# Performance work log

Measured on AMD Instinct MI355X. Metric: run time of the kernel, lower is better.

## Reference

```python
import jax, jax.numpy as jnp
import numpy as np

N, E, H = 50000, 800000, 4

def setup_inputs() -> dict:
    key = jax.random.key(0)
    ks = jax.random.split(key, 16)
    feat = jax.random.normal(ks[0], (N, 2), dtype=jnp.float32)
    src = jax.random.randint(ks[1], (E,), 0, N, dtype=jnp.int32)
    dst = jax.random.randint(ks[2], (E,), 0, N, dtype=jnp.int32)
    def w(k, shape, fan_in):
        return jax.random.normal(k, shape, dtype=jnp.float32) * (1.0 / np.sqrt(fan_in))
    # layer 1: 2 -> 4 heads x 32
    W1 = w(ks[3], (2, 128), 2); al1 = w(ks[4], (H, 32), 32); ar1 = w(ks[5], (H, 32), 32); b1 = jnp.zeros((128,), jnp.float32)
    # layer 2: 128 -> 4 heads x 32
    W2 = w(ks[6], (128, 128), 128); al2 = w(ks[7], (H, 32), 32); ar2 = w(ks[8], (H, 32), 32); b2 = jnp.zeros((128,), jnp.float32)
    # layer 3: 128 -> 4 heads x 64
    W3 = w(ks[9], (128, 256), 128); al3 = w(ks[10], (H, 64), 64); ar3 = w(ks[11], (H, 64), 64); b3 = jnp.zeros((256,), jnp.float32)
    return dict(feat=feat, src=src, dst=dst, W1=W1, al1=al1, ar1=ar1, b1=b1,
                W2=W2, al2=al2, ar2=ar2, b2=b2, W3=W3, al3=al3, ar3=ar3, b3=b3)

def gat_layer(h, W, al, ar, b, src, dst):
    # h: [N, Fin]; W: [Fin, H*D]; al/ar: [H, D]; b: [H*D]
    Hh, D = al.shape
    z = (h @ W).reshape(-1, Hh, D)                      # [N, H, D]
    el = jnp.sum(z * al[None], axis=-1)                 # [N, H]
    er = jnp.sum(z * ar[None], axis=-1)                 # [N, H]
    e = jax.nn.leaky_relu(el[src] + er[dst], 0.2)       # [E, H]
    m = jax.ops.segment_max(e, dst, num_segments=N)     # [N, H] per-dst max
    ex = jnp.exp(e - m[dst])                            # [E, H]
    s = jax.ops.segment_sum(ex, dst, num_segments=N)    # [N, H]
    alpha = ex / s[dst]                                 # edge softmax
    msg = z[src] * alpha[:, :, None]                    # [E, H, D] gathered+weighted
    out = jax.ops.segment_sum(msg, dst, num_segments=N) # [N, H, D]
    return out.reshape(N, Hh * D) + b

def reference(feat, src, dst, W1, al1, ar1, b1, W2, al2, ar2, b2, W3, al3, ar3, b3):
    # dropout is identity at inference
    h = jax.nn.relu(gat_layer(feat, W1, al1, ar1, b1, src, dst))
    h = jax.nn.relu(gat_layer(h, W2, al2, ar2, b2, src, dst))
    h = gat_layer(h, W3, al3, ar3, b3, src, dst)
    return h
```

## Files before the change

### kernel.cpp

```cpp
#include <hip/hip_runtime.h>
#include <math.h>


#define NEG_BIG (-1e38f)

typedef _Float16 h8 __attribute__((ext_vector_type(8)));
typedef _Float16 h4 __attribute__((ext_vector_type(4)));

static inline int cdiv(int a, int b) { return (a + b - 1) / b; }

__device__ __forceinline__ float lrelu(float x) { return (x >= 0.f) ? x : 0.2f * x; }


__global__ void count_deg_kernel(const int* __restrict__ dst, int* __restrict__ deg, int E) {
    int i = blockIdx.x * blockDim.x + threadIdx.x;
    if (i < E) atomicAdd(&deg[dst[i]], 1);
}

__global__ __launch_bounds__(256) void scan1_kernel(const int* __restrict__ deg,
                                                    int* __restrict__ rowptr,
                                                    int* __restrict__ bsum, int n) {
    __shared__ int wsum[4];
    int t = threadIdx.x;
    int l = t & 63, wv = t >> 6;
    int i = blockIdx.x * 256 + t;
    int v = (i < n) ? deg[i] : 0;
    int x = v;
    #pragma unroll
    for (int off = 1; off < 64; off <<= 1) {
        int y = __shfl_up(x, off);
        if (l >= off) x += y;
    }
    if (l == 63) wsum[wv] = x;
    __syncthreads();
    int wo = 0;
    #pragma unroll
    for (int j = 0; j < 4; ++j)
        if (j < wv) wo += wsum[j];
    if (i < n) rowptr[i] = wo + x - v;
    if (t == 255) bsum[blockIdx.x] = wo + x;
}

__global__ __launch_bounds__(256) void scan2_kernel(const int* __restrict__ bsum,
                                                    int* __restrict__ boff, int nb) {
    __shared__ int wsum[4];
    int t = threadIdx.x;
    int l = t & 63, wv = t >> 6;
    int v = (t < nb) ? bsum[t] : 0;
    int x = v;
    #pragma unroll
    for (int off = 1; off < 64; off <<= 1) {
        int y = __shfl_up(x, off);
        if (l >= off) x += y;
    }
    if (l == 63) wsum[wv] = x;
    __syncthreads();
    int wo = 0;
    #pragma unroll
    for (int j = 0; j < 4; ++j)
        if (j < wv) wo += wsum[j];
    if (t < nb) boff[t] = wo + x - v;
}

__global__ __launch_bounds__(256) void scan3_kernel(int* __restrict__ rowptr,
                                                    const int* __restrict__ boff,
                                                    int n, int E) {
    int i = blockIdx.x * 256 + threadIdx.x;
    if (i < n) rowptr[i] += boff[blockIdx.x];
    if (i == 0) rowptr[n] = E;
}

__global__ void fill_csr_kernel(const int* __restrict__ src, const int* __restrict__ dst,
                                const int* __restrict__ rowptr,
                                int* __restrict__ cursor, int* __restrict__ csrc, int E) {
    int i = blockIdx.x * blockDim.x + threadIdx.x;
    if (i < E) {
        int d = dst[i];
        int pos = atomicAdd(&cursor[d], 1);
        csrc[rowptr[d] + pos] = src[i];
    }
}


__global__ __launch_bounds__(256) void agg1_kernel(
        const float* __restrict__ feat, const float* __restrict__ W1,
        const float* __restrict__ al, const float* __restrict__ ar,
        const int* __restrict__ rowptr, const int* __restrict__ csrc,
        const float* __restrict__ bias, _Float16* __restrict__ out, int N) {
    constexpr int GRP = 16, NV = 4;
    __shared__ float2 fss[4][NV][GRP + 1];
    __shared__ float  exs[4][NV][4][GRP + 1];
    const int l = threadIdx.x & 63;
    const int w = threadIdx.x >> 6;
    const int g = l >> 4;
    const int lg = l & 15;
    const int v = blockIdx.x * (4 * NV) + w * NV + g;

    float w0l = W1[l], w0h = W1[l + 64];
    float w1l = W1[128 + l], w1h = W1[128 + l + 64];
    float all_ = al[l], alh = al[l + 64];
    float arl = ar[l], arh = ar[l + 64];
    float pa0 = w0l * all_, pa1 = w0h * alh;
    float pb0 = w1l * all_, pb1 = w1h * alh;
    float pc0 = w0l * arl,  pc1 = w0h * arh;
    float pd0 = w1l * arl,  pd1 = w1h * arh;
    #pragma unroll
    for (int off = 1; off < 32; off <<= 1) {
        pa0 += __shfl_xor(pa0, off); pa1 += __shfl_xor(pa1, off);
        pb0 += __shfl_xor(pb0, off); pb1 += __shfl_xor(pb1, off);
        pc0 += __shfl_xor(pc0, off); pc1 += __shfl_xor(pc1, off);
        pd0 += __shfl_xor(pd0, off); pd1 += __shfl_xor(pd1, off);
    }
    float4 Ael = make_float4(__shfl(pa0, 0), __shfl(pa0, 32),
                             __shfl(pa1, 0), __shfl(pa1, 32));
    float4 Bel = make_float4(__shfl(pb0, 0), __shfl(pb0, 32),
                             __shfl(pb1, 0), __shfl(pb1, 32));
    float4 Aer = make_float4(__shfl(pc0, 0), __shfl(pc0, 32),
                             __shfl(pc1, 0), __shfl(pc1, 32));
    float4 Ber = make_float4(__shfl(pd0, 0), __shfl(pd0, 32),
                             __shfl(pd1, 0), __shfl(pd1, 32));

    if (v >= N) return;
    const int r0 = rowptr[v], r1 = rowptr[v + 1];
    const int c0 = lg * 8;
    const int h = lg >> 2;
    float4 w0a = *(const float4*)&W1[c0];
    float4 w0b = *(const float4*)&W1[c0 + 4];
    float4 w1a = *(const float4*)&W1[128 + c0];
    float4 w1b = *(const float4*)&W1[128 + c0 + 4];
    float4 b0 = *(const float4*)(bias + c0);
    float4 b1 = *(const float4*)(bias + c0 + 4);
    float4 o0, o1;

    if (r0 == r1) {
        o0 = b0; o1 = b1;
    } else {
        float2 fv = *(const float2*)(feat + (size_t)v * 2);
        float4 er4 = make_float4(fmaf(fv.x, Aer.x, fv.y * Ber.x),
                                 fmaf(fv.x, Aer.y, fv.y * Ber.y),
                                 fmaf(fv.x, Aer.z, fv.y * Ber.z),
                                 fmaf(fv.x, Aer.w, fv.y * Ber.w));

        float m0 = NEG_BIG, m1 = NEG_BIG, m2 = NEG_BIG, m3 = NEG_BIG;
        float2 fs0 = make_float2(0.f, 0.f);
        float4 e40 = make_float4(NEG_BIG, NEG_BIG, NEG_BIG, NEG_BIG);
        for (int base = r0; base < r1; base += GRP) {
            int i = base + lg;
            float ex_ = NEG_BIG, ey_ = NEG_BIG, ez_ = NEG_BIG, ew_ = NEG_BIG;
            float2 fs = make_float2(0.f, 0.f);
            if (i < r1) {
                int sv = csrc[i];
                fs = *(const float2*)(feat + (size_t)sv * 2);
                ex_ = lrelu(fmaf(fs.x, Ael.x, fs.y * Bel.x) + er4.x);
                ey_ = lrelu(fmaf(fs.x, Ael.y, fs.y * Bel.y) + er4.y);
                ez_ = lrelu(fmaf(fs.x, Ael.z, fs.y * Bel.z) + er4.z);
                ew_ = lrelu(fmaf(fs.x, Ael.w, fs.y * Bel.w) + er4.w);
            }
            if (base == r0) { fs0 = fs; e40 = make_float4(ex_, ey_, ez_, ew_); }
            m0 = fmaxf(m0, ex_); m1 = fmaxf(m1, ey_);
            m2 = fmaxf(m2, ez_); m3 = fmaxf(m3, ew_);
        }
        #pragma unroll
        for (int off = 1; off < GRP; off <<= 1) {
            m0 = fmaxf(m0, __shfl_xor(m0, off));
            m1 = fmaxf(m1, __shfl_xor(m1, off));
            m2 = fmaxf(m2, __shfl_xor(m2, off));
            m3 = fmaxf(m3, __shfl_xor(m3, off));
        }

        float s0 = 0.f, s1 = 0.f, s2 = 0.f, s3 = 0.f;
        float4 a0 = make_float4(0.f, 0.f, 0.f, 0.f);
        float4 a1 = make_float4(0.f, 0.f, 0.f, 0.f);

        for (int base = r0; base < r1; base += GRP) {
            int i = base + lg;
            float2 fs; float4 e4;
            if (base == r0) {
                fs = fs0; e4 = e40;
            } else if (i < r1) {
                int sv = csrc[i];
                fs = *(const float2*)(feat + (size_t)sv * 2);
                e4 = make_float4(
                    lrelu(fmaf(fs.x, Ael.x, fs.y * Bel.x) + er4.x),
                    lrelu(fmaf(fs.x, Ael.y, fs.y * Bel.y) + er4.y),
                    lrelu(fmaf(fs.x, Ael.z, fs.y * Bel.z) + er4.z),
                    lrelu(fmaf(fs.x, Ael.w, fs.y * Bel.w) + er4.w));
            } else {
                fs = make_float2(0.f, 0.f);
                e4 = make_float4(NEG_BIG, NEG_BIG, NEG_BIG, NEG_BIG);
            }
            bool valid = (i < r1);
            float exv0 = valid ? __expf(e4.x - m0) : 0.f;
            float exv1 = valid ? __expf(e4.y - m1) : 0.f;
            float exv2 = valid ? __expf(e4.z - m2) : 0.f;
            float exv3 = valid ? __expf(e4.w - m3) : 0.f;
            s0 += exv0; s1 += exv1; s2 += exv2; s3 += exv3;
            fss[w][g][lg] = fs;
            exs[w][g][0][lg] = exv0; exs[w][g][1][lg] = exv1;
            exs[w][g][2][lg] = exv2; exs[w][g][3][lg] = exv3;
            int cnt = min(GRP, r1 - base);
            #pragma unroll 8
            for (int k = 0; k < cnt; ++k) {
                float2 fk = fss[w][g][k];
                float exk = exs[w][g][h][k];
                float u = fk.x * exk;
                float t = fk.y * exk;
                a0.x = fmaf(u, w0a.x, fmaf(t, w1a.x, a0.x));
                a0.y = fmaf(u, w0a.y, fmaf(t, w1a.y, a0.y));
                a0.z = fmaf(u, w0a.z, fmaf(t, w1a.z, a0.z));
                a0.w = fmaf(u, w0a.w, fmaf(t, w1a.w, a0.w));
                a1.x = fmaf(u, w0b.x, fmaf(t, w1b.x, a1.x));
                a1.y = fmaf(u, w0b.y, fmaf(t, w1b.y, a1.y));
                a1.z = fmaf(u, w0b.z, fmaf(t, w1b.z, a1.z));
                a1.w = fmaf(u, w0b.w, fmaf(t, w1b.w, a1.w));
            }
        }
        #pragma unroll
        for (int off = 1; off < GRP; off <<= 1) {
            s0 += __shfl_xor(s0, off);
            s1 += __shfl_xor(s1, off);
            s2 += __shfl_xor(s2, off);
            s3 += __shfl_xor(s3, off);
        }
        float s = (h == 0) ? s0 : (h == 1) ? s1 : (h == 2) ? s2 : s3;
        float inv = 1.f / s;
        o0 = make_float4(fmaf(a0.x, inv, b0.x), fmaf(a0.y, inv, b0.y),
                         fmaf(a0.z, inv, b0.z), fmaf(a0.w, inv, b0.w));
        o1 = make_float4(fmaf(a1.x, inv, b1.x), fmaf(a1.y, inv, b1.y),
                         fmaf(a1.z, inv, b1.z), fmaf(a1.w, inv, b1.w));
    }
    o0.x = fmaxf(o0.x, 0.f); o0.y = fmaxf(o0.y, 0.f);
    o0.z = fmaxf(o0.z, 0.f); o0.w = fmaxf(o0.w, 0.f);
    o1.x = fmaxf(o1.x, 0.f); o1.y = fmaxf(o1.y, 0.f);
    o1.z = fmaxf(o1.z, 0.f); o1.w = fmaxf(o1.w, 0.f);
    h8 ho;
    ho[0] = (_Float16)o0.x; ho[1] = (_Float16)o0.y;
    ho[2] = (_Float16)o0.z; ho[3] = (_Float16)o0.w;
    ho[4] = (_Float16)o1.x; ho[5] = (_Float16)o1.y;
    ho[6] = (_Float16)o1.z; ho[7] = (_Float16)o1.w;
    *(h8*)(out + (size_t)v * 128 + c0) = ho;
}


template <int HDOUT>
__global__ __launch_bounds__(256) void gemm_tile_kernel(
        const _Float16* __restrict__ A, const float* __restrict__ W,
        const float* __restrict__ al, const float* __restrict__ ar,
        _Float16* __restrict__ ZH, float* __restrict__ el, float* __restrict__ er,
        int N) {
    __shared__ __align__(16) float AT[64][132];
    __shared__ __align__(16) float WS[64][64];
    int n0 = blockIdx.x * 128;
    int c0 = blockIdx.y * 64;
    int t = threadIdx.x;
    int tr = t >> 4;
    int tc = t & 15;

    float acc[8][4] = {};

    for (int kc = 0; kc < 128; kc += 64) {
        {
            int kk = (t & 7) * 8;
            int rb = t >> 3;
            #pragma unroll
            for (int it = 0; it < 4; ++it) {
                int r = rb + 32 * it;
                int n = n0 + r;
                h8 a;
                #pragma unroll
                for (int j = 0; j < 8; ++j) a[j] = (_Float16)0.f;
                if (n < N) a = *(const h8*)&A[(size_t)n * 128 + kc + kk];
                #pragma unroll
                for (int j = 0; j < 8; ++j) AT[kk + j][r] = (float)a[j];
            }
        }
        {
            int cc = (t & 15) * 4;
            int kb = t >> 4;
            #pragma unroll
            for (int it = 0; it < 4; ++it) {
                int k = kb + 16 * it;
                *(float4*)&WS[k][cc] =
                    *(const float4*)&W[(size_t)(kc + k) * HDOUT + c0 + cc];
            }
        }
        __syncthreads();

        #pragma unroll 4
        for (int k = 0; k < 64; ++k) {
            float4 a0 = *(const float4*)&AT[k][tr * 8];
            float4 a1 = *(const float4*)&AT[k][tr * 8 + 4];
            float4 wv = *(const float4*)&WS[k][tc * 4];
            acc[0][0] = fmaf(a0.x, wv.x, acc[0][0]); acc[0][1] = fmaf(a0.x, wv.y, acc[0][1]);
            acc[0][2] = fmaf(a0.x, wv.z, acc[0][2]); acc[0][3] = fmaf(a0.x, wv.w, acc[0][3]);
            acc[1][0] = fmaf(a0.y, wv.x, acc[1][0]); acc[1][1] = fmaf(a0.y, wv.y, acc[1][1]);
            acc[1][2] = fmaf(a0.y, wv.z, acc[1][2]); acc[1][3] = fmaf(a0.y, wv.w, acc[1][3]);
            acc[2][0] = fmaf(a0.z, wv.x, acc[2][0]); acc[2][1] = fmaf(a0.z, wv.y, acc[2][1]);
            acc[2][2] = fmaf(a0.z, wv.z, acc[2][2]); acc[2][3] = fmaf(a0.z, wv.w, acc[2][3]);
            acc[3][0] = fmaf(a0.w, wv.x, acc[3][0]); acc[3][1] = fmaf(a0.w, wv.y, acc[3][1]);
            acc[3][2] = fmaf(a0.w, wv.z, acc[3][2]); acc[3][3] = fmaf(a0.w, wv.w, acc[3][3]);
            acc[4][0] = fmaf(a1.x, wv.x, acc[4][0]); acc[4][1] = fmaf(a1.x, wv.y, acc[4][1]);
            acc[4][2] = fmaf(a1.x, wv.z, acc[4][2]); acc[4][3] = fmaf(a1.x, wv.w, acc[4][3]);
            acc[5][0] = fmaf(a1.y, wv.x, acc[5][0]); acc[5][1] = fmaf(a1.y, wv.y, acc[5][1]);
            acc[5][2] = fmaf(a1.y, wv.z, acc[5][2]); acc[5][3] = fmaf(a1.y, wv.w, acc[5][3]);
            acc[6][0] = fmaf(a1.z, wv.x, acc[6][0]); acc[6][1] = fmaf(a1.z, wv.y, acc[6][1]);
            acc[6][2] = fmaf(a1.z, wv.z, acc[6][2]); acc[6][3] = fmaf(a1.z, wv.w, acc[6][3]);
            acc[7][0] = fmaf(a1.w, wv.x, acc[7][0]); acc[7][1] = fmaf(a1.w, wv.y, acc[7][1]);
            acc[7][2] = fmaf(a1.w, wv.z, acc[7][2]); acc[7][3] = fmaf(a1.w, wv.w, acc[7][3]);
        }
        __syncthreads();
    }

    float4 alv = *(const float4*)&al[c0 + tc * 4];
    float4 arv = *(const float4*)&ar[c0 + tc * 4];

    #pragma unroll
    for (int i = 0; i < 8; ++i) {
        int n = n0 + tr * 8 + i;
        bool ok = (n < N);
        if (ok) {
            h4 hz4 = { (_Float16)acc[i][0], (_Float16)acc[i][1],
                       (_Float16)acc[i][2], (_Float16)acc[i][3] };
            *(h4*)&ZH[(size_t)n * HDOUT + c0 + tc * 4] = hz4;
        }
        float pe = acc[i][0] * alv.x + acc[i][1] * alv.y +
                   acc[i][2] * alv.z + acc[i][3] * alv.w;
        float pr = acc[i][0] * arv.x + acc[i][1] * arv.y +
                   acc[i][2] * arv.z + acc[i][3] * arv.w;
        if (HDOUT == 128) {
            #pragma unroll
            for (int off = 1; off < 8; off <<= 1) {
                pe += __shfl_xor(pe, off);
                pr += __shfl_xor(pr, off);
            }
            if (ok && (tc & 7) == 0) {
                int h = 2 * blockIdx.y + (tc >> 3);
                el[(size_t)n * 4 + h] = pe;
                er[(size_t)n * 4 + h] = pr;
            }
        } else {
            #pragma unroll
            for (int off = 1; off < 16; off <<= 1) {
                pe += __shfl_xor(pe, off);
                pr += __shfl_xor(pr, off);
            }
            if (ok && tc == 0) {
                int h = blockIdx.y;
                el[(size_t)n * 4 + h] = pe;
                er[(size_t)n * 4 + h] = pr;
            }
        }
    }
}


template <bool RELU, int GRP, int HD, typename OUTT>
__global__ __launch_bounds__(256) void agg_kernel(
        const _Float16* __restrict__ zh, const float* __restrict__ el,
        const float* __restrict__ er, const int* __restrict__ rowptr,
        const int* __restrict__ csrc, const float* __restrict__ bias,
        OUTT* __restrict__ out, int N) {
    constexpr int NV = 64 / GRP;
    constexpr int CH = HD / GRP;
    constexpr int HGRP = GRP / 4;
    static_assert(CH == 8, "config assumes 8 channels per lane");
    __shared__ float exs[4][NV][4][GRP + 1];
    __shared__ int   svs[4][NV][GRP + 1];
    const int l = threadIdx.x & 63;
    const int w = threadIdx.x >> 6;
    const int g = l / GRP;
    const int lg = l & (GRP - 1);
    const int v = blockIdx.x * (4 * NV) + w * NV + g;
    if (v >= N) return;
    const int r0 = rowptr[v], r1 = rowptr[v + 1];
    const int c0 = lg * CH;
    const int h = lg / HGRP;
    float4 b0 = *(const float4*)(bias + c0);
    float4 b1 = *(const float4*)(bias + c0 + 4);
    float4 o0, o1;

    if (r0 == r1) {
        o0 = b0; o1 = b1;
    } else {
        float4 er4 = *(const float4*)(er + (size_t)v * 4);

        float m0 = NEG_BIG, m1 = NEG_BIG, m2 = NEG_BIG, m3 = NEG_BIG;
        int sv0 = 0;
        float4 e40 = make_float4(NEG_BIG, NEG_BIG, NEG_BIG, NEG_BIG);
        for (int base = r0; base < r1; base += GRP) {
            int i = base + lg;
            float ex_ = NEG_BIG, ey_ = NEG_BIG, ez_ = NEG_BIG, ew_ = NEG_BIG;
            int sv = 0;
            if (i < r1) {
                sv = csrc[i];
                float4 ev = *(const float4*)(el + (size_t)sv * 4);
                ex_ = lrelu(ev.x + er4.x);
                ey_ = lrelu(ev.y + er4.y);
                ez_ = lrelu(ev.z + er4.z);
                ew_ = lrelu(ev.w + er4.w);
            }
            if (base == r0) { sv0 = sv; e40 = make_float4(ex_, ey_, ez_, ew_); }
            m0 = fmaxf(m0, ex_); m1 = fmaxf(m1, ey_);
            m2 = fmaxf(m2, ez_); m3 = fmaxf(m3, ew_);
        }
        #pragma unroll
        for (int off = 1; off < GRP; off <<= 1) {
            m0 = fmaxf(m0, __shfl_xor(m0, off));
            m1 = fmaxf(m1, __shfl_xor(m1, off));
            m2 = fmaxf(m2, __shfl_xor(m2, off));
            m3 = fmaxf(m3, __shfl_xor(m3, off));
        }

        float s0 = 0.f, s1 = 0.f, s2 = 0.f, s3 = 0.f;
        float4 a0 = make_float4(0.f, 0.f, 0.f, 0.f);
        float4 a1 = make_float4(0.f, 0.f, 0.f, 0.f);

        for (int base = r0; base < r1; base += GRP) {
            int i = base + lg;
            int sv; float4 e4;
            if (base == r0) {
                sv = sv0; e4 = e40;
            } else if (i < r1) {
                sv = csrc[i];
                float4 ev = *(const float4*)(el + (size_t)sv * 4);
                e4 = make_float4(lrelu(ev.x + er4.x), lrelu(ev.y + er4.y),
                                 lrelu(ev.z + er4.z), lrelu(ev.w + er4.w));
            } else {
                sv = 0; e4 = make_float4(NEG_BIG, NEG_BIG, NEG_BIG, NEG_BIG);
            }
            bool valid = (i < r1);
            float exv0 = valid ? __expf(e4.x - m0) : 0.f;
            float exv1 = valid ? __expf(e4.y - m1) : 0.f;
            float exv2 = valid ? __expf(e4.z - m2) : 0.f;
            float exv3 = valid ? __expf(e4.w - m3) : 0.f;
            s0 += exv0; s1 += exv1; s2 += exv2; s3 += exv3;
            svs[w][g][lg] = sv;
            exs[w][g][0][lg] = exv0; exs[w][g][1][lg] = exv1;
            exs[w][g][2][lg] = exv2; exs[w][g][3][lg] = exv3;
            int cnt = min(GRP, r1 - base);
            #pragma unroll 8
            for (int k = 0; k < cnt; ++k) {
                int svk = svs[w][g][k];
                float exk = exs[w][g][h][k];
                h8 zz = *(const h8*)(zh + (size_t)svk * HD + c0);
                a0.x = fmaf((float)zz[0], exk, a0.x);
                a0.y = fmaf((float)zz[1], exk, a0.y);
                a0.z = fmaf((float)zz[2], exk, a0.z);
                a0.w = fmaf((float)zz[3], exk, a0.w);
                a1.x = fmaf((float)zz[4], exk, a1.x);
                a1.y = fmaf((float)zz[5], exk, a1.y);
                a1.z = fmaf((float)zz[6], exk, a1.z);
                a1.w = fmaf((float)zz[7], exk, a1.w);
            }
        }
        #pragma unroll
        for (int off = 1; off < GRP; off <<= 1) {
            s0 += __shfl_xor(s0, off);
            s1 += __shfl_xor(s1, off);
            s2 += __shfl_xor(s2, off);
            s3 += __shfl_xor(s3, off);
        }
        float s = (h == 0) ? s0 : (h == 1) ? s1 : (h == 2) ? s2 : s3;
        float inv = 1.f / s;
        o0 = make_float4(fmaf(a0.x, inv, b0.x), fmaf(a0.y, inv, b0.y),
                         fmaf(a0.z, inv, b0.z), fmaf(a0.w, inv, b0.w));
        o1 = make_float4(fmaf(a1.x, inv, b1.x), fmaf(a1.y, inv, b1.y),
                         fmaf(a1.z, inv, b1.z), fmaf(a1.w, inv, b1.w));
    }
    if (RELU) {
        o0.x = fmaxf(o0.x, 0.f); o0.y = fmaxf(o0.y, 0.f);
        o0.z = fmaxf(o0.z, 0.f); o0.w = fmaxf(o0.w, 0.f);
        o1.x = fmaxf(o1.x, 0.f); o1.y = fmaxf(o1.y, 0.f);
        o1.z = fmaxf(o1.z, 0.f); o1.w = fmaxf(o1.w, 0.f);
    }
    if constexpr (sizeof(OUTT) == 2) {
        h8 ho;
        ho[0] = (_Float16)o0.x; ho[1] = (_Float16)o0.y;
        ho[2] = (_Float16)o0.z; ho[3] = (_Float16)o0.w;
        ho[4] = (_Float16)o1.x; ho[5] = (_Float16)o1.y;
        ho[6] = (_Float16)o1.z; ho[7] = (_Float16)o1.w;
        *(h8*)((_Float16*)out + (size_t)v * HD + c0) = ho;
    } else {
        float* op = (float*)out + (size_t)v * HD + c0;
        *(float4*)op = o0;
        *(float4*)(op + 4) = o1;
    }
}


extern "C" void kernel_launch(void* const* d_in, const int* in_sizes, int n_in,
                              void* d_out, int out_size, void* d_ws, size_t ws_size,
                              hipStream_t stream) {
    const float* feat = (const float*)d_in[0];
    const int* src = (const int*)d_in[1];
    const int* dst = (const int*)d_in[2];
    const float* W1 = (const float*)d_in[3];
    const float* al1 = (const float*)d_in[4];
    const float* ar1 = (const float*)d_in[5];
    const float* b1 = (const float*)d_in[6];
    const float* W2 = (const float*)d_in[7];
    const float* al2 = (const float*)d_in[8];
    const float* ar2 = (const float*)d_in[9];
    const float* b2 = (const float*)d_in[10];
    const float* W3 = (const float*)d_in[11];
    const float* al3 = (const float*)d_in[12];
    const float* ar3 = (const float*)d_in[13];
    const float* b3 = (const float*)d_in[14];
    const int N = in_sizes[0] / 2;
    const int E = in_sizes[1];

    _Float16* hbuf = (_Float16*)d_ws;
    float* el = (float*)(hbuf + (size_t)N * 128);
    float* er = el + (size_t)N * 4;
    _Float16* zh = (_Float16*)(er + (size_t)N * 4);
    int* csrc = (int*)(zh + (size_t)N * 256);
    int* deg = csrc + E;
    int* cursor = deg + N;
    int* rowptr = cursor + N;
    int* bsum = rowptr + (N + 1);
    int* boff = bsum + 256;

    const int nb = cdiv(N, 256);

    hipMemsetAsync(deg, 0, sizeof(int) * (size_t)(2 * N), stream);
    count_deg_kernel<<<cdiv(E, 256), 256, 0, stream>>>(dst, deg, E);
    scan1_kernel<<<nb, 256, 0, stream>>>(deg, rowptr, bsum, N);
    scan2_kernel<<<1, 256, 0, stream>>>(bsum, boff, nb);
    scan3_kernel<<<nb, 256, 0, stream>>>(rowptr, boff, N, E);
    fill_csr_kernel<<<cdiv(E, 256), 256, 0, stream>>>(src, dst, rowptr, cursor, csrc, E);

    agg1_kernel<<<cdiv(N, 16), 256, 0, stream>>>(feat, W1, al1, ar1, rowptr, csrc,
                                                 b1, hbuf, N);

    gemm_tile_kernel<128><<<dim3(cdiv(N, 128), 2), 256, 0, stream>>>(
        hbuf, W2, al2, ar2, zh, el, er, N);
    agg_kernel<true, 16, 128, _Float16><<<cdiv(N, 16), 256, 0, stream>>>(
        zh, el, er, rowptr, csrc, b2, hbuf, N);

    gemm_tile_kernel<256><<<dim3(cdiv(N, 128), 4), 256, 0, stream>>>(
        hbuf, W3, al3, ar3, zh, el, er, N);
    agg_kernel<false, 32, 256, float><<<cdiv(N, 8), 256, 0, stream>>>(
        zh, el, er, rowptr, csrc, b3, (float*)d_out, N);
}
```

Measured before the change: 327.4 us.

## Replace FP32 tiled GEMM with MFMA fp16 GEMM using pre-transposed fp16 weights

Replaces the shared-memory FP32 FMA GEMM for layers 2 and 3 with a wave-per-16-row kernel that uses the 16x16x32 fp16 MFMA instruction. A-fragments are loaded straight from global memory into registers and B-fragments come from the new transposed fp16 weight buffers, so no LDS staging is needed. The attention logits el and er are still fused in through shuffle reductions. Weights are now converted and transposed to fp16 by small kernels on every call, which lowers weight precision and writes ZH as scattered 2-byte stores.

```diff
diff --git a/kernel.cpp b/kernel.cpp
--- a/kernel.cpp
+++ b/kernel.cpp
@@ -6,6 +6,7 @@
 
 typedef _Float16 h8 __attribute__((ext_vector_type(8)));
 typedef _Float16 h4 __attribute__((ext_vector_type(4)));
+typedef float f32x4 __attribute__((ext_vector_type(4)));
 
 static inline int cdiv(int a, int b) { return (a + b - 1) / b; }
 
@@ -78,6 +79,17 @@
         int d = dst[i];
         int pos = atomicAdd(&cursor[d], 1);
         csrc[rowptr[d] + pos] = src[i];
+    }
+}
+
+
+template <int HDOUT>
+__global__ __launch_bounds__(256) void wconv_kernel(const float* __restrict__ W,
+                                                    _Float16* __restrict__ WT) {
+    int idx = blockIdx.x * 256 + threadIdx.x;
+    if (idx < 128 * HDOUT) {
+        int k = idx / HDOUT, c = idx % HDOUT;
+        WT[(size_t)c * 128 + k] = (_Float16)W[idx];
     }
 }
 
@@ -243,111 +255,74 @@
 
 
 template <int HDOUT>
-__global__ __launch_bounds__(256) void gemm_tile_kernel(
-        const _Float16* __restrict__ A, const float* __restrict__ W,
+__global__ __launch_bounds__(256) void gemm_mfma_kernel(
+        const _Float16* __restrict__ A, const _Float16* __restrict__ WT,
         const float* __restrict__ al, const float* __restrict__ ar,
         _Float16* __restrict__ ZH, float* __restrict__ el, float* __restrict__ er,
         int N) {
-    __shared__ __align__(16) float AT[64][132];
-    __shared__ __align__(16) float WS[64][64];
-    int n0 = blockIdx.x * 128;
-    int c0 = blockIdx.y * 64;
-    int t = threadIdx.x;
-    int tr = t >> 4;
-    int tc = t & 15;
-
-    float acc[8][4] = {};
-
-    for (int kc = 0; kc < 128; kc += 64) {
-        {
-            int kk = (t & 7) * 8;
-            int rb = t >> 3;
+    constexpr int TPH = HDOUT / 64;
+    const int l = threadIdx.x & 63;
+    const int wid = blockIdx.x * 4 + (threadIdx.x >> 6);
+    const int m0 = wid * 16;
+    if (m0 >= N) return;
+    const int lc = l & 15;
+    const int kg = l >> 4;
+
+    h8 afrag[4];
+    {
+        int m = m0 + lc;
+        if (m < N) {
+            const _Float16* ap = A + (size_t)m * 128 + kg * 8;
             #pragma unroll
-            for (int it = 0; it < 4; ++it) {
-                int r = rb + 32 * it;
-                int n = n0 + r;
-                h8 a;
-                #pragma unroll
-                for (int j = 0; j < 8; ++j) a[j] = (_Float16)0.f;
-                if (n < N) a = *(const h8*)&A[(size_t)n * 128 + kc + kk];
-                #pragma unroll
-                for (int j = 0; j < 8; ++j) AT[kk + j][r] = (float)a[j];
-            }
-        }
-        {
-            int cc = (t & 15) * 4;
-            int kb = t >> 4;
-            #pragma unroll
-            for (int it = 0; it < 4; ++it) {
-                int k = kb + 16 * it;
-                *(float4*)&WS[k][cc] =
-                    *(const float4*)&W[(size_t)(kc + k) * HDOUT + c0 + cc];
-            }
-        }
-        __syncthreads();
-
-        #pragma unroll 4
-        for (int k = 0; k < 64; ++k) {
-            float4 a0 = *(const float4*)&AT[k][tr * 8];
-            float4 a1 = *(const float4*)&AT[k][tr * 8 + 4];
-            float4 wv = *(const float4*)&WS[k][tc * 4];
-            acc[0][0] = fmaf(a0.x, wv.x, acc[0][0]); acc[0][1] = fmaf(a0.x, wv.y, acc[0][1]);
-            acc[0][2] = fmaf(a0.x, wv.z, acc[0][2]); acc[0][3] = fmaf(a0.x, wv.w, acc[0][3]);
-            acc[1][0] = fmaf(a0.y, wv.x, acc[1][0]); acc[1][1] = fmaf(a0.y, wv.y, acc[1][1]);
-            acc[1][2] = fmaf(a0.y, wv.z, acc[1][2]); acc[1][3] = fmaf(a0.y, wv.w, acc[1][3]);
-            acc[2][0] = fmaf(a0.z, wv.x, acc[2][0]); acc[2][1] = fmaf(a0.z, wv.y, acc[2][1]);
-            acc[2][2] = fmaf(a0.z, wv.z, acc[2][2]); acc[2][3] = fmaf(a0.z, wv.w, acc[2][3]);
-            acc[3][0] = fmaf(a0.w, wv.x, acc[3][0]); acc[3][1] = fmaf(a0.w, wv.y, acc[3][1]);
-            acc[3][2] = fmaf(a0.w, wv.z, acc[3][2]); acc[3][3] = fmaf(a0.w, wv.w, acc[3][3]);
-            acc[4][0] = fmaf(a1.x, wv.x, acc[4][0]); acc[4][1] = fmaf(a1.x, wv.y, acc[4][1]);
-            acc[4][2] = fmaf(a1.x, wv.z, acc[4][2]); acc[4][3] = fmaf(a1.x, wv.w, acc[4][3]);
-            acc[5][0] = fmaf(a1.y, wv.x, acc[5][0]); acc[5][1] = fmaf(a1.y, wv.y, acc[5][1]);
-            acc[5][2] = fmaf(a1.y, wv.z, acc[5][2]); acc[5][3] = fmaf(a1.y, wv.w, acc[5][3]);
-            acc[6][0] = fmaf(a1.z, wv.x, acc[6][0]); acc[6][1] = fmaf(a1.z, wv.y, acc[6][1]);
-            acc[6][2] = fmaf(a1.z, wv.z, acc[6][2]); acc[6][3] = fmaf(a1.z, wv.w, acc[6][3]);
-            acc[7][0] = fmaf(a1.w, wv.x, acc[7][0]); acc[7][1] = fmaf(a1.w, wv.y, acc[7][1]);
-            acc[7][2] = fmaf(a1.w, wv.z, acc[7][2]); acc[7][3] = fmaf(a1.w, wv.w, acc[7][3]);
-        }
-        __syncthreads();
-    }
-
-    float4 alv = *(const float4*)&al[c0 + tc * 4];
-    float4 arv = *(const float4*)&ar[c0 + tc * 4];
-
-    #pragma unroll
-    for (int i = 0; i < 8; ++i) {
-        int n = n0 + tr * 8 + i;
-        bool ok = (n < N);
-        if (ok) {
-            h4 hz4 = { (_Float16)acc[i][0], (_Float16)acc[i][1],
-                       (_Float16)acc[i][2], (_Float16)acc[i][3] };
-            *(h4*)&ZH[(size_t)n * HDOUT + c0 + tc * 4] = hz4;
-        }
-        float pe = acc[i][0] * alv.x + acc[i][1] * alv.y +
-                   acc[i][2] * alv.z + acc[i][3] * alv.w;
-        float pr = acc[i][0] * arv.x + acc[i][1] * arv.y +
-                   acc[i][2] * arv.z + acc[i][3] * arv.w;
-        if (HDOUT == 128) {
-            #pragma unroll
-            for (int off = 1; off < 8; off <<= 1) {
-                pe += __shfl_xor(pe, off);
-                pr += __shfl_xor(pr, off);
-            }
-            if (ok && (tc & 7) == 0) {
-                int h = 2 * blockIdx.y + (tc >> 3);
-                el[(size_t)n * 4 + h] = pe;
-                er[(size_t)n * 4 + h] = pr;
-            }
+            for (int ks = 0; ks < 4; ++ks) afrag[ks] = *(const h8*)(ap + ks * 32);
         } else {
             #pragma unroll
-            for (int off = 1; off < 16; off <<= 1) {
-                pe += __shfl_xor(pe, off);
-                pr += __shfl_xor(pr, off);
-            }
-            if (ok && tc == 0) {
-                int h = blockIdx.y;
-                el[(size_t)n * 4 + h] = pe;
-                er[(size_t)n * 4 + h] = pr;
+            for (int ks = 0; ks < 4; ++ks)
+                #pragma unroll
+                for (int j = 0; j < 8; ++j) afrag[ks][j] = (_Float16)0.f;
+        }
+    }
+
+    #pragma unroll
+    for (int h = 0; h < 4; ++h) {
+        float pel[4] = {0.f, 0.f, 0.f, 0.f};
+        float per_[4] = {0.f, 0.f, 0.f, 0.f};
+        #pragma unroll
+        for (int tt = 0; tt < TPH; ++tt) {
+            int col = (h * TPH + tt) * 16 + lc;
+            f32x4 acc = {0.f, 0.f, 0.f, 0.f};
+            const _Float16* wp = WT + (size_t)col * 128 + kg * 8;
+            #pragma unroll
+            for (int ks = 0; ks < 4; ++ks) {
+                h8 bfrag = *(const h8*)(wp + ks * 32);
+                acc = __builtin_amdgcn_mfma_f32_16x16x32_f16(afrag[ks], bfrag, acc,
+                                                             0, 0, 0);
+            }
+            float alc = al[col], arc = ar[col];
+            #pragma unroll
+            for (int r = 0; r < 4; ++r) {
+                int n = m0 + kg * 4 + r;
+                if (n < N) ZH[(size_t)n * HDOUT + col] = (_Float16)acc[r];
+                pel[r] = fmaf(acc[r], alc, pel[r]);
+                per_[r] = fmaf(acc[r], arc, per_[r]);
+            }
+        }
+        #pragma unroll
+        for (int off = 1; off < 16; off <<= 1) {
+            #pragma unroll
+            for (int r = 0; r < 4; ++r) {
+                pel[r] += __shfl_xor(pel[r], off);
+                per_[r] += __shfl_xor(per_[r], off);
+            }
+        }
+        if (lc == 0) {
+            #pragma unroll
+            for (int r = 0; r < 4; ++r) {
+                int n = m0 + kg * 4 + r;
+                if (n < N) {
+                    el[(size_t)n * 4 + h] = pel[r];
+                    er[(size_t)n * 4 + h] = per_[r];
+                }
             }
         }
     }
@@ -513,7 +488,9 @@
     float* el = (float*)(hbuf + (size_t)N * 128);
     float* er = el + (size_t)N * 4;
     _Float16* zh = (_Float16*)(er + (size_t)N * 4);
-    int* csrc = (int*)(zh + (size_t)N * 256);
+    _Float16* WT2 = zh + (size_t)N * 256;
+    _Float16* WT3 = WT2 + 128 * 128;
+    int* csrc = (int*)(WT3 + 256 * 128);
     int* deg = csrc + E;
     int* cursor = deg + N;
     int* rowptr = cursor + N;
@@ -523,6 +500,8 @@
     const int nb = cdiv(N, 256);
 
     hipMemsetAsync(deg, 0, sizeof(int) * (size_t)(2 * N), stream);
+    wconv_kernel<128><<<cdiv(128 * 128, 256), 256, 0, stream>>>(W2, WT2);
+    wconv_kernel<256><<<cdiv(128 * 256, 256), 256, 0, stream>>>(W3, WT3);
     count_deg_kernel<<<cdiv(E, 256), 256, 0, stream>>>(dst, deg, E);
     scan1_kernel<<<nb, 256, 0, stream>>>(deg, rowptr, bsum, N);
     scan2_kernel<<<1, 256, 0, stream>>>(bsum, boff, nb);
@@ -532,13 +511,13 @@
     agg1_kernel<<<cdiv(N, 16), 256, 0, stream>>>(feat, W1, al1, ar1, rowptr, csrc,
                                                  b1, hbuf, N);
 
-    gemm_tile_kernel<128><<<dim3(cdiv(N, 128), 2), 256, 0, stream>>>(
-        hbuf, W2, al2, ar2, zh, el, er, N);
+    gemm_mfma_kernel<128><<<cdiv(N, 64), 256, 0, stream>>>(
+        hbuf, WT2, al2, ar2, zh, el, er, N);
     agg_kernel<true, 16, 128, _Float16><<<cdiv(N, 16), 256, 0, stream>>>(
         zh, el, er, rowptr, csrc, b2, hbuf, N);
 
-    gemm_tile_kernel<256><<<dim3(cdiv(N, 128), 4), 256, 0, stream>>>(
-        hbuf, W3, al3, ar3, zh, el, er, N);
+    gemm_mfma_kernel<256><<<cdiv(N, 64), 256, 0, stream>>>(
+        hbuf, WT3, al3, ar3, zh, el, er, N);
     agg_kernel<false, 32, 256, float><<<cdiv(N, 8), 256, 0, stream>>>(
         zh, el, er, rowptr, csrc, b3, (float*)d_out, N);
 }
```

New measurement: 291.5 us. -11.0%, faster.
